# Kernel tuning notes

Measured on AMD Instinct MI355X. Metric: run time of the kernel, lower is better.

## Reference

```python
import jax, jax.numpy as jnp
import numpy as np

DEPTH = 4  # truncation depth of the signature


def setup_inputs() -> dict:
    key = jax.random.key(0)
    # (N, L, C) batch of paths
    path = jax.random.normal(key, (32, 256, 8), dtype=jnp.float32)
    return {"path": path}


def _signature(path, depth):
    """Truncated path signature via Chen's relation over linear segments.

    For a linear segment with increment dx, its signature is exp(dx) in the
    tensor algebra: level j = dx^{\otimes j} / j!.  The signature of the
    concatenated path is the tensor-algebra product of segment signatures,
    computed with a scan over segments.
    """
    N, L, C = path.shape
    dx = path[:, 1:, :] - path[:, :-1, :]  # (N, L-1, C) increments

    def exp_levels(d):
        # levels of exp(d): e_j = d^{\otimes j} / j!, flattened to (N, C^j)
        levels = [d]
        for j in range(2, depth + 1):
            nxt = jnp.einsum('na,nb->nab', levels[-1], d).reshape(N, -1) / j
            levels.append(nxt)
        return levels

    def step(carry, d):
        # carry: tuple of (N, C^k) for k = 1..depth (levels of running signature)
        # Chen: new_k = sum_{i+j=k} carry_i (x) e_j, with carry_0 = e_0 = 1
        e = exp_levels(d)
        new = []
        for k in range(1, depth + 1):
            acc = carry[k - 1] + e[k - 1]  # i=k,j=0 and i=0,j=k terms
            for i in range(1, k):
                acc = acc + jnp.einsum(
                    'na,nb->nab', carry[i - 1], e[k - i - 1]
                ).reshape(N, -1)
            new.append(acc)
        return tuple(new), None

    init = tuple(jnp.zeros((N, C ** k), path.dtype) for k in range(1, depth + 1))
    final, _ = jax.lax.scan(step, init, jnp.swapaxes(dx, 0, 1))  # scan over L-1
    return jnp.concatenate(final, axis=-1)  # (N, C + C^2 + ... + C^depth)


def reference(path):
    return _signature(path, DEPTH)
```

## Files before the change

kernel.cpp:

```cpp
#include <hip/hip_runtime.h>

#define NBATCH 32
#define NSEG 255
#define SIGLEN 4680
#define INV6 (1.0f/6.0f)
#define INV24 (1.0f/24.0f)

typedef float v2f __attribute__((ext_vector_type(2)));

__global__ __launch_bounds__(512)
__attribute__((amdgpu_waves_per_eu(2, 2)))
void sig_kernel(const float* __restrict__ path, float* __restrict__ out) {
    const int n = blockIdx.x;
    const int t = threadIdx.x;
    const int w = t >> 6, l = t & 63, a = l >> 3, b = l & 7;

    __shared__ float pbuf[2048];
    __shared__ float dbuf[2048];
    __shared__ float r1buf[2048];
    __shared__ float WS[8][64];
    __shared__ float PB[4][36 * 128];

    const float* prow = path + n * 2048;
    { const int i4 = t * 4; *(float4*)&pbuf[i4] = *(const float4*)&prow[i4]; }
    __syncthreads();
    {
        const int i4 = t * 4;
        if (i4 < NSEG * 8) {
            const float4 xv0 = *(const float4*)&pbuf[i4];
            const float4 xv1 = *(const float4*)&pbuf[i4 + 8];
            *(float4*)&dbuf[i4] = make_float4(xv1.x - xv0.x, xv1.y - xv0.y,
                                              xv1.z - xv0.z, xv1.w - xv0.w);
            const float4 xt = *(const float4*)&pbuf[2040 + (i4 & 4)];
            *(float4*)&r1buf[i4] = make_float4(xt.x - xv1.x, xt.y - xv1.y,
                                               xt.z - xv1.z, xt.w - xv1.w);
        } else {
            *(float4*)&dbuf[i4]  = make_float4(0.f, 0.f, 0.f, 0.f);
            *(float4*)&r1buf[i4] = make_float4(0.f, 0.f, 0.f, 0.f);
        }
    }
    __syncthreads();

    {
        float xh = pbuf[(w << 8) + a] - pbuf[a];
        float wsum = 0.f;
        #pragma unroll 8
        for (int k = (w << 5); k < (w << 5) + 32; ++k) {
            const float da = dbuf[k * 8 + a], db = dbuf[k * 8 + b];
            wsum = fmaf(db, fmaf(0.5f, da, xh), wsum);
            xh += da;
        }
        WS[w][l] = wsum;
    }
    __syncthreads();

    float S2w = 0.f;
    for (int m = 0; m < w; ++m) S2w += WS[m][l];
    float S1a = pbuf[(w << 8) + a] - pbuf[a];

    v2f C[32];
    v2f S3C[4];
    #pragma unroll
    for (int j = 0; j < 32; ++j) C[j] = (v2f)0.f;
    #pragma unroll
    for (int j = 0; j < 4; ++j) S3C[j] = (v2f)0.f;

    const int jstart = w << 5;
    #pragma unroll 4
    for (int ss = 0; ss < 32; ++ss) {
        const int j = jstart + ss;
        const v2f dp[4] = {*(const v2f*)&dbuf[j * 8 + 0],
                           *(const v2f*)&dbuf[j * 8 + 2],
                           *(const v2f*)&dbuf[j * 8 + 4],
                           *(const v2f*)&dbuf[j * 8 + 6]};
        const v2f rp[4] = {*(const v2f*)&r1buf[j * 8 + 0],
                           *(const v2f*)&r1buf[j * 8 + 2],
                           *(const v2f*)&r1buf[j * 8 + 4],
                           *(const v2f*)&r1buf[j * 8 + 6]};
        const float da = dbuf[j * 8 + a], db = dbuf[j * 8 + b];
        const float dab = da * db;
        const float sdb = S1a * db;
        const float Q = fmaf(dab, INV6,  fmaf(sdb, 0.5f, S2w));
        const float P = fmaf(dab, INV24, fmaf(sdb, INV6, 0.5f * S2w));
        const v2f Qv = Q, Pv = P;
        v2f E[4];
        #pragma unroll
        for (int eh = 0; eh < 4; ++eh)
            E[eh] = __builtin_elementwise_fma(Qv, rp[eh], Pv * dp[eh]);
        const float dcs[8] = {dp[0].x, dp[0].y, dp[1].x, dp[1].y,
                              dp[2].x, dp[2].y, dp[3].x, dp[3].y};
        #pragma unroll
        for (int c = 0; c < 8; ++c) {
            const v2f dcv = dcs[c];
            #pragma unroll
            for (int eh = 0; eh < 4; ++eh)
                C[c * 4 + eh] = __builtin_elementwise_fma(dcv, E[eh], C[c * 4 + eh]);
        }
        #pragma unroll
        for (int ch = 0; ch < 4; ++ch)
            S3C[ch] = __builtin_elementwise_fma(Qv, dp[ch], S3C[ch]);
        S2w = fmaf(db, fmaf(0.5f, da, S1a), S2w);
        S1a += da;
    }

    #pragma unroll
    for (int r = 0; r < 3; ++r) {
        const int stride = 1 << r;
        const int m = (stride << 1) - 1;
        const int buf = w >> (r + 1);
        if ((w & m) == stride) {
            #pragma unroll
            for (int s = 0; s < 32; ++s)
                *(v2f*)&PB[buf][s * 128 + 2 * l] = C[s];
            #pragma unroll
            for (int ch = 0; ch < 4; ++ch)
                *(v2f*)&PB[buf][(32 + ch) * 128 + 2 * l] = S3C[ch];
        }
        __syncthreads();
        if ((w & m) == 0) {
            #pragma unroll
            for (int s = 0; s < 32; ++s)
                C[s] += *(const v2f*)&PB[buf][s * 128 + 2 * l];
            #pragma unroll
            for (int ch = 0; ch < 4; ++ch)
                S3C[ch] += *(const v2f*)&PB[buf][(32 + ch) * 128 + 2 * l];
        }
        __syncthreads();
    }

    if (w == 0) {
        float* o = out + n * SIGLEN;
        if (b == 0) o[a] = pbuf[2040 + a] - pbuf[a];
        {
            float s2 = WS[0][l];
            #pragma unroll
            for (int m2 = 1; m2 < 8; ++m2) s2 += WS[m2][l];
            o[8 + l] = s2;
        }
        *(float4*)&o[72 + l * 8]     = make_float4(S3C[0].x, S3C[0].y, S3C[1].x, S3C[1].y);
        *(float4*)&o[72 + l * 8 + 4] = make_float4(S3C[2].x, S3C[2].y, S3C[3].x, S3C[3].y);
        #pragma unroll
        for (int c = 0; c < 8; ++c) {
            *(float4*)&o[584 + l * 64 + c * 8] =
                make_float4(C[c*4+0].x, C[c*4+0].y, C[c*4+1].x, C[c*4+1].y);
            *(float4*)&o[584 + l * 64 + c * 8 + 4] =
                make_float4(C[c*4+2].x, C[c*4+2].y, C[c*4+3].x, C[c*4+3].y);
        }
    }
}

extern "C" void kernel_launch(void* const* d_in, const int* in_sizes, int n_in,
                              void* d_out, int out_size, void* d_ws, size_t ws_size,
                              hipStream_t stream) {
    const float* path = (const float*)d_in[0];
    float* out = (float*)d_out;
    sig_kernel<<<NBATCH, 512, 0, stream>>>(path, out);
}
```

Baseline: 18.57 us.

## Split each batch's segment scan across eight blocks with last-block global reduction

Each path is now processed by eight workgroups, each covering 32 segments with 4 per wave, instead of one workgroup per path. The level-2 prefix is computed from 64 per-4-segment partial sums. Each block writes its partial level-3/4 sums to workspace with agent-scope atomic stores, and the last block to arrive (tracked by an atomic counter) sums the eight partials into the output. This raises the grid from 32 to 256 blocks to fill more compute units, at the cost of global round-trips, an extra memset launch, and relaxed-ordering synchronization that relies on an explicit s_waitcnt.

Result: slower. 27.75 us (+49.5%).

```diff
diff --git a/kernel.cpp b/kernel.cpp
--- a/kernel.cpp
+++ b/kernel.cpp
@@ -3,23 +3,28 @@
 #define NBATCH 32
 #define NSEG 255
 #define SIGLEN 4680
+#define PSTR 4608
 #define INV6 (1.0f/6.0f)
 #define INV24 (1.0f/24.0f)
 
 typedef float v2f __attribute__((ext_vector_type(2)));
+typedef unsigned long long u64;
 
 __global__ __launch_bounds__(512)
 __attribute__((amdgpu_waves_per_eu(2, 2)))
-void sig_kernel(const float* __restrict__ path, float* __restrict__ out) {
-    const int n = blockIdx.x;
+void sig_kernel(const float* __restrict__ path, float* __restrict__ pbase,
+                int* __restrict__ flags, float* __restrict__ out) {
+    const int blk = blockIdx.x;
+    const int n = blk >> 3, cb = blk & 7;
     const int t = threadIdx.x;
     const int w = t >> 6, l = t & 63, a = l >> 3, b = l & 7;
 
     __shared__ float pbuf[2048];
     __shared__ float dbuf[2048];
     __shared__ float r1buf[2048];
-    __shared__ float WS[8][64];
+    __shared__ float WSS[64][64];
     __shared__ float PB[4][36 * 128];
+    __shared__ int sh_old;
 
     const float* prow = path + n * 2048;
     { const int i4 = t * 4; *(float4*)&pbuf[i4] = *(const float4*)&prow[i4]; }
@@ -41,22 +46,25 @@
     }
     __syncthreads();
 
-    {
-        float xh = pbuf[(w << 8) + a] - pbuf[a];
-        float wsum = 0.f;
-        #pragma unroll 8
-        for (int k = (w << 5); k < (w << 5) + 32; ++k) {
+    const float x0a = pbuf[a];
+
+    #pragma unroll
+    for (int s8 = 0; s8 < 8; ++s8) {
+        const int s = 8 * w + s8;
+        float acc = 0.f;
+        #pragma unroll
+        for (int k = 4 * s; k < 4 * s + 4; ++k) {
             const float da = dbuf[k * 8 + a], db = dbuf[k * 8 + b];
-            wsum = fmaf(db, fmaf(0.5f, da, xh), wsum);
-            xh += da;
+            const float xa = pbuf[k * 8 + a] - x0a;
+            acc = fmaf(db, fmaf(0.5f, da, xa), acc);
         }
-        WS[w][l] = wsum;
+        WSS[s][l] = acc;
     }
     __syncthreads();
 
     float S2w = 0.f;
-    for (int m = 0; m < w; ++m) S2w += WS[m][l];
-    float S1a = pbuf[(w << 8) + a] - pbuf[a];
+    const int npre = 8 * cb + w;
+    for (int s = 0; s < npre; ++s) S2w += WSS[s][l];
 
     v2f C[32];
     v2f S3C[4];
@@ -65,10 +73,10 @@
     #pragma unroll
     for (int j = 0; j < 4; ++j) S3C[j] = (v2f)0.f;
 
-    const int jstart = w << 5;
-    #pragma unroll 4
-    for (int ss = 0; ss < 32; ++ss) {
-        const int j = jstart + ss;
+    const int j0 = cb * 32 + 4 * w;
+    #pragma unroll
+    for (int ss = 0; ss < 4; ++ss) {
+        const int j = j0 + ss;
         const v2f dp[4] = {*(const v2f*)&dbuf[j * 8 + 0],
                            *(const v2f*)&dbuf[j * 8 + 2],
                            *(const v2f*)&dbuf[j * 8 + 4],
@@ -78,6 +86,7 @@
                            *(const v2f*)&r1buf[j * 8 + 4],
                            *(const v2f*)&r1buf[j * 8 + 6]};
         const float da = dbuf[j * 8 + a], db = dbuf[j * 8 + b];
+        const float S1a = pbuf[j * 8 + a] - x0a;
         const float dab = da * db;
         const float sdb = S1a * db;
         const float Q = fmaf(dab, INV6,  fmaf(sdb, 0.5f, S2w));
@@ -100,7 +109,6 @@
         for (int ch = 0; ch < 4; ++ch)
             S3C[ch] = __builtin_elementwise_fma(Qv, dp[ch], S3C[ch]);
         S2w = fmaf(db, fmaf(0.5f, da, S1a), S2w);
-        S1a += da;
     }
 
     #pragma unroll
@@ -110,8 +118,7 @@
         const int buf = w >> (r + 1);
         if ((w & m) == stride) {
             #pragma unroll
-            for (int s = 0; s < 32; ++s)
-                *(v2f*)&PB[buf][s * 128 + 2 * l] = C[s];
+            for (int s = 0; s < 32; ++s) *(v2f*)&PB[buf][s * 128 + 2 * l] = C[s];
             #pragma unroll
             for (int ch = 0; ch < 4; ++ch)
                 *(v2f*)&PB[buf][(32 + ch) * 128 + 2 * l] = S3C[ch];
@@ -119,8 +126,7 @@
         __syncthreads();
         if ((w & m) == 0) {
             #pragma unroll
-            for (int s = 0; s < 32; ++s)
-                C[s] += *(const v2f*)&PB[buf][s * 128 + 2 * l];
+            for (int s = 0; s < 32; ++s) C[s] += *(const v2f*)&PB[buf][s * 128 + 2 * l];
             #pragma unroll
             for (int ch = 0; ch < 4; ++ch)
                 S3C[ch] += *(const v2f*)&PB[buf][(32 + ch) * 128 + 2 * l];
@@ -129,22 +135,52 @@
     }
 
     if (w == 0) {
-        float* o = out + n * SIGLEN;
-        if (b == 0) o[a] = pbuf[2040 + a] - pbuf[a];
-        {
-            float s2 = WS[0][l];
+        float* p = pbase + (size_t)blk * PSTR;
+        #pragma unroll
+        for (int ch = 0; ch < 4; ++ch) {
+            u64 uv; __builtin_memcpy(&uv, &S3C[ch], 8);
+            __hip_atomic_store((u64*)&p[l * 8 + 2 * ch], uv,
+                               __ATOMIC_RELAXED, __HIP_MEMORY_SCOPE_AGENT);
+        }
+        #pragma unroll
+        for (int c = 0; c < 8; ++c)
             #pragma unroll
-            for (int m2 = 1; m2 < 8; ++m2) s2 += WS[m2][l];
+            for (int eh = 0; eh < 4; ++eh) {
+                u64 uv; __builtin_memcpy(&uv, &C[c * 4 + eh], 8);
+                __hip_atomic_store((u64*)&p[512 + l * 64 + c * 8 + 2 * eh], uv,
+                                   __ATOMIC_RELAXED, __HIP_MEMORY_SCOPE_AGENT);
+            }
+        if (cb == 0) {
+            float* o = out + n * SIGLEN;
+            if (b == 0) o[a] = pbuf[2040 + a] - pbuf[a];
+            float s2 = WSS[0][l];
+            #pragma unroll
+            for (int s = 1; s < 64; ++s) s2 += WSS[s][l];
             o[8 + l] = s2;
         }
-        *(float4*)&o[72 + l * 8]     = make_float4(S3C[0].x, S3C[0].y, S3C[1].x, S3C[1].y);
-        *(float4*)&o[72 + l * 8 + 4] = make_float4(S3C[2].x, S3C[2].y, S3C[3].x, S3C[3].y);
-        #pragma unroll
-        for (int c = 0; c < 8; ++c) {
-            *(float4*)&o[584 + l * 64 + c * 8] =
-                make_float4(C[c*4+0].x, C[c*4+0].y, C[c*4+1].x, C[c*4+1].y);
-            *(float4*)&o[584 + l * 64 + c * 8 + 4] =
-                make_float4(C[c*4+2].x, C[c*4+2].y, C[c*4+3].x, C[c*4+3].y);
+        asm volatile("s_waitcnt vmcnt(0)" ::: "memory");
+    }
+    __syncthreads();
+    if (t == 0)
+        sh_old = __hip_atomic_fetch_add(&flags[n], 1, __ATOMIC_RELAXED,
+                                        __HIP_MEMORY_SCOPE_AGENT);
+    __syncthreads();
+    if (sh_old != 7) return;
+
+    {
+        float* o = out + n * SIGLEN;
+        const u64* p0 = (const u64*)(pbase + (size_t)(n * 8) * PSTR);
+        for (int i = t; i < PSTR / 2; i += 512) {
+            v2f sum = (v2f)0.f;
+            #pragma unroll
+            for (int pi = 0; pi < 8; ++pi) {
+                u64 uv = __hip_atomic_load(&p0[(size_t)pi * (PSTR / 2) + i],
+                                           __ATOMIC_RELAXED,
+                                           __HIP_MEMORY_SCOPE_AGENT);
+                v2f v; __builtin_memcpy(&v, &uv, 8);
+                sum += v;
+            }
+            *(v2f*)&o[72 + 2 * i] = sum;
         }
     }
 }
@@ -154,5 +190,8 @@
                               hipStream_t stream) {
     const float* path = (const float*)d_in[0];
     float* out = (float*)d_out;
-    sig_kernel<<<NBATCH, 512, 0, stream>>>(path, out);
+    int* flags = (int*)d_ws;
+    float* pbase = (float*)d_ws + 256;
+    hipMemsetAsync(d_ws, 0, NBATCH * sizeof(int), stream);
+    sig_kernel<<<NBATCH * 8, 512, 0, stream>>>(path, pbase, flags, out);
 }
```
